# Kernel tuning notes

Measured on AMD Instinct MI355X. Metric: run time of the kernel, lower is better.

## Reference

```python
import jax, jax.numpy as jnp
import numpy as np

QUERY_DIM = 3072
HEADS = 24
HEAD_DIM = 128
INNER = HEADS * HEAD_DIM  # 3072
MLP_HIDDEN = int(QUERY_DIM * 4.0)  # 12288
MLP_MULT = 2
EPS = 1e-5
B, S = 1, 4096


def setup_inputs() -> dict:
    key = jax.random.key(0)
    ks = jax.random.split(key, 8)
    hidden_states = jax.random.normal(ks[0], (B, S, QUERY_DIM), dtype=jnp.float32)
    # rotary angles for half the head dim (interleaved / non-neox style)
    t = jnp.arange(S, dtype=jnp.float32)[:, None]
    inv_freq = 1.0 / (10000.0 ** (jnp.arange(0, HEAD_DIM, 2, dtype=jnp.float32) / HEAD_DIM))
    ang = t * inv_freq[None, :]
    cos = jnp.cos(ang)
    sin = jnp.sin(ang)
    W_qkv_mlp = jax.random.normal(ks[1], (QUERY_DIM, 3 * INNER + MLP_HIDDEN * MLP_MULT), dtype=jnp.float32) * 0.02
    W_out = jax.random.normal(ks[2], (INNER + MLP_HIDDEN, QUERY_DIM), dtype=jnp.float32) * 0.02
    b_out = jnp.zeros((QUERY_DIM,), dtype=jnp.float32)
    norm_q_w = jnp.ones((HEAD_DIM,), dtype=jnp.float32)
    norm_k_w = jnp.ones((HEAD_DIM,), dtype=jnp.float32)
    return {"hidden_states": hidden_states, "cos": cos, "sin": sin,
            "W_qkv_mlp": W_qkv_mlp, "W_out": W_out, "b_out": b_out,
            "norm_q_w": norm_q_w, "norm_k_w": norm_k_w}


def _rmsnorm(x, w, eps=EPS):
    var = jnp.mean(jnp.square(x), axis=-1, keepdims=True)
    return x * jax.lax.rsqrt(var + eps) * w


def _rope_interleaved(x, cos, sin):
    # x: [B,S,H,D]; cos/sin: [S, D//2]. Non-neox: rotate interleaved pairs.
    x1 = x[..., 0::2]
    x2 = x[..., 1::2]
    c = cos[None, :, None, :]
    s = sin[None, :, None, :]
    o1 = x1 * c - x2 * s
    o2 = x2 * c + x1 * s
    return jnp.stack([o1, o2], axis=-1).reshape(x.shape)


def reference(hidden_states, cos, sin, W_qkv_mlp, W_out, b_out, norm_q_w, norm_k_w):
    h = hidden_states @ W_qkv_mlp  # [B,S, 3*INNER + 2*MLP_HIDDEN]
    qkv, mlp = jnp.split(h, [3 * INNER], axis=-1)
    q, k, v = jnp.split(qkv, 3, axis=-1)
    q = q.reshape(B, S, HEADS, HEAD_DIM)
    k = k.reshape(B, S, HEADS, HEAD_DIM)
    v = v.reshape(B, S, HEADS, HEAD_DIM)
    q = _rmsnorm(q, norm_q_w)
    k = _rmsnorm(k, norm_k_w)
    q = _rope_interleaved(q, cos, sin)
    k = _rope_interleaved(k, cos, sin)
    scale = 1.0 / np.sqrt(HEAD_DIM)
    scores = jnp.einsum('bqhd,bkhd->bhqk', q, k) * scale
    probs = jax.nn.softmax(scores, axis=-1)
    attn = jnp.einsum('bhqk,bkhd->bqhd', probs, v)
    attn = attn.reshape(B, S, INNER)
    m1, m2 = jnp.split(mlp, 2, axis=-1)
    mlp_out = jax.nn.silu(m1) * m2
    out = jnp.concatenate([attn, mlp_out], axis=-1) @ W_out + b_out
    return out
```

## Files before the change

### kernel.cpp

```cpp
#include <hip/hip_runtime.h>

typedef short shortx8 __attribute__((ext_vector_type(8)));
typedef float floatx4 __attribute__((ext_vector_type(4)));
typedef unsigned short u16;

#define GLB(x) ((const __attribute__((address_space(1))) void*)(x))
#define LDSC(x) ((__attribute__((address_space(3))) void*)(x))
#define BAR() asm volatile("s_barrier" ::: "memory")
#define WAITV8() asm volatile("s_waitcnt vmcnt(8)" ::: "memory")

__device__ __forceinline__ float bf2f(u16 u) {
  unsigned x = ((unsigned)u) << 16;
  float f;
  __builtin_memcpy(&f, &x, 4);
  return f;
}
__device__ __forceinline__ u16 f2bf(float f) {
  unsigned x;
  __builtin_memcpy(&x, &f, 4);
  x += 0x7fffu + ((x >> 16) & 1u);
  return (u16)(x >> 16);
}

__global__ __launch_bounds__(256) void cast_bf16(const float* __restrict__ src,
                                                 u16* __restrict__ dst) {
  const size_t i = ((size_t)blockIdx.x * 256 + threadIdx.x) << 3;
  floatx4 a = *(const floatx4*)(src + i);
  floatx4 b = *(const floatx4*)(src + i + 4);
  shortx8 o;
#pragma unroll
  for (int e = 0; e < 4; ++e) {
    o[e] = (short)f2bf(a[e]);
    o[e + 4] = (short)f2bf(b[e]);
  }
  *(shortx8*)(dst + i) = o;
}

__global__ __launch_bounds__(256) void transpose_cast(const float* __restrict__ src,
                                                      u16* __restrict__ dst,
                                                      int R, int C, int perm) {
  __shared__ u16 T[64 * 72];
  const int tiles_c = C >> 6;
  const int r0 = (blockIdx.x / tiles_c) << 6;
  const int c0 = (blockIdx.x % tiles_c) << 6;
  const int tid = threadIdx.x;
  const int rl = tid >> 4;
  const int cb = (tid & 15) << 2;
#pragma unroll
  for (int rr = 0; rr < 4; ++rr) {
    const int row = rr * 16 + rl;
    floatx4 v = *(const floatx4*)(src + (size_t)(r0 + row) * C + c0 + cb);
#pragma unroll
    for (int i = 0; i < 4; ++i) T[(cb + i) * 72 + row] = f2bf(v[i]);
  }
  __syncthreads();
  int dbase = c0;
  if (perm && c0 >= 9216) {
    if (c0 < 21504) { const int u = c0 - 9216;  dbase = 9216 + ((u >> 7) << 8) + (u & 64); }
    else            { const int u = c0 - 21504; dbase = 9216 + ((u >> 7) << 8) + 128 + (u & 64); }
  }
#pragma unroll
  for (int ii = 0; ii < 2; ++ii) {
    const int chunk = tid + (ii << 8);
    const int cr = chunk >> 3;
    const int r8 = (chunk & 7) << 3;
    shortx8 v = *(const shortx8*)(T + cr * 72 + r8);
    *(shortx8*)(dst + (size_t)(dbase + cr) * R + r0 + r8) = v;
  }
}

template <int MODE>
__global__ __launch_bounds__(512, 2) void gemm8(const u16* __restrict__ A,
                                                const u16* __restrict__ B,
                                                void* __restrict__ Cout,
                                                u16* __restrict__ CC2,
                                                int M, int N, int K, int Ksub) {
  __shared__ u16 lds[8 * 8192];

  const int nbm = M >> 8;
  const int nwg = nbm * (N >> 8);
  const int cpx = nwg >> 3;
  const int wg = ((int)blockIdx.x & 7) * cpx + ((int)blockIdx.x >> 3);
  const int bm = wg % nbm;
  const int bn = wg / nbm;
  const int koff = (int)blockIdx.y * Ksub;

  const int tid = threadIdx.x;
  const int lane = tid & 63;
  const int w = tid >> 6;
  const int wm = w >> 2;
  const int wn = w & 3;
  const int l15 = lane & 15;
  const int l4 = lane >> 4;
  const int NT = Ksub >> 6;

  const int lrow = lane >> 2;
  const int lblk = lane & 3;

#define UNIT(buf, mat, ks) (lds + (((buf) * 4 + (mat) * 2 + (ks)) << 13))

  const u16* Abase = A + (size_t)bm * 256 * K + koff;
  const u16* Bbase = B + (size_t)bn * 256 * K + koff;

  auto STAGE = [&](int mat, int ks, int buf, int t) {
    const u16* gb = mat ? Bbase : Abase;
#pragma unroll
    for (int j = 0; j < 2; ++j) {
      const int row = (w * 2 + j) * 16 + lrow;
      const int sblk = lblk ^ ((row >> 1) & 3);
      const u16* src = gb + (size_t)row * K + (t << 6) + (ks << 5) + (sblk << 3);
      __builtin_amdgcn_global_load_lds(GLB(src),
                                       LDSC(UNIT(buf, mat, ks) + ((w * 2 + j) << 9)),
                                       16, 0, 0);
    }
  };
  auto LDA = [&](int mf, int ks, int buf) -> shortx8 {
    const int row = wm * 128 + mf * 16 + l15;
    return *(const shortx8*)(UNIT(buf, 0, ks) + row * 32 + ((l4 ^ ((row >> 1) & 3)) << 3));
  };
  auto LDB = [&](int nf, int ks, int buf) -> shortx8 {
    const int row = wn * 64 + nf * 16 + l15;
    return *(const shortx8*)(UNIT(buf, 1, ks) + row * 32 + ((l4 ^ ((row >> 1) & 3)) << 3));
  };

  floatx4 acc[8][4] = {};

  STAGE(0, 0, 0, 0); STAGE(1, 0, 0, 0);
  STAGE(0, 1, 0, 0); STAGE(1, 1, 0, 0);
  STAGE(0, 0, 1, 1); STAGE(1, 0, 1, 1);
  WAITV8();
  BAR();

#pragma unroll 2
  for (int T = 0; T < NT; ++T) {
    const int cur = T & 1, nxt = cur ^ 1;
    const int t1 = (T + 1 < NT) ? T + 1 : NT - 1;
    const int t2 = (T + 2 < NT) ? T + 2 : NT - 1;
    shortx8 af[4], bf[4];

#pragma unroll
    for (int m = 0; m < 4; ++m) af[m] = LDA(m, 0, cur);
#pragma unroll
    for (int n = 0; n < 4; ++n) bf[n] = LDB(n, 0, cur);
    STAGE(0, 1, nxt, t1);
    BAR();
    __builtin_amdgcn_s_setprio(1);
#pragma unroll
    for (int m = 0; m < 4; ++m)
#pragma unroll
      for (int n = 0; n < 4; ++n)
        acc[m][n] = __builtin_amdgcn_mfma_f32_16x16x32_bf16(af[m], bf[n], acc[m][n], 0, 0, 0);
    __builtin_amdgcn_s_setprio(0);
    BAR();

#pragma unroll
    for (int m = 0; m < 4; ++m) af[m] = LDA(4 + m, 0, cur);
    STAGE(1, 1, nxt, t1);
    BAR();
    __builtin_amdgcn_s_setprio(1);
#pragma unroll
    for (int m = 0; m < 4; ++m)
#pragma unroll
      for (int n = 0; n < 4; ++n)
        acc[4 + m][n] = __builtin_amdgcn_mfma_f32_16x16x32_bf16(af[m], bf[n], acc[4 + m][n], 0, 0, 0);
    __builtin_amdgcn_s_setprio(0);
    WAITV8();
    BAR();

#pragma unroll
    for (int m = 0; m < 4; ++m) af[m] = LDA(m, 1, cur);
#pragma unroll
    for (int n = 0; n < 4; ++n) bf[n] = LDB(n, 1, cur);
    STAGE(0, 0, cur, t2);
    BAR();
    __builtin_amdgcn_s_setprio(1);
#pragma unroll
    for (int m = 0; m < 4; ++m)
#pragma unroll
      for (int n = 0; n < 4; ++n)
        acc[m][n] = __builtin_amdgcn_mfma_f32_16x16x32_bf16(af[m], bf[n], acc[m][n], 0, 0, 0);
    __builtin_amdgcn_s_setprio(0);
    BAR();

#pragma unroll
    for (int m = 0; m < 4; ++m) af[m] = LDA(4 + m, 1, cur);
    STAGE(1, 0, cur, t2);
    BAR();
    __builtin_amdgcn_s_setprio(1);
#pragma unroll
    for (int m = 0; m < 4; ++m)
#pragma unroll
      for (int n = 0; n < 4; ++n)
        acc[4 + m][n] = __builtin_amdgcn_mfma_f32_16x16x32_bf16(af[m], bf[n], acc[4 + m][n], 0, 0, 0);
    __builtin_amdgcn_s_setprio(0);
    WAITV8();
    BAR();
  }

  const int orow0 = bm * 256 + wm * 128 + (l4 << 2);
  if (MODE == 0) {
    if (bn < 36) {
      u16* C = (u16*)Cout;
      const int ocol0 = bn * 256 + wn * 64 + l15;
#pragma unroll
      for (int m = 0; m < 8; ++m)
#pragma unroll
        for (int n = 0; n < 4; ++n)
#pragma unroll
          for (int r = 0; r < 4; ++r)
            C[(size_t)(orow0 + m * 16 + r) * 9216 + ocol0 + n * 16] = f2bf(acc[m][n][r]);
    } else {
      __syncthreads();
      float* buf = (float*)lds + (wm * 2 + (wn & 1)) * 8192;
      if (wn >= 2) {
#pragma unroll
        for (int m = 0; m < 8; ++m)
#pragma unroll
          for (int n = 0; n < 4; ++n) {
            const int col = n * 16 + l15;
            const int chunk = (m * 4 + l4) ^ (l15 & 7);
            *(floatx4*)(buf + ((col << 5) + chunk) * 4) = acc[m][n];
          }
      }
      __syncthreads();
      if (wn < 2) {
        const int gcol0 = 3072 + (bn - 36) * 128 + wn * 64 + l15;
#pragma unroll
        for (int m = 0; m < 8; ++m)
#pragma unroll
          for (int n = 0; n < 4; ++n) {
            const int col = n * 16 + l15;
            const int chunk = (m * 4 + l4) ^ (l15 & 7);
            const floatx4 m2v = *(const floatx4*)(buf + ((col << 5) + chunk) * 4);
#pragma unroll
            for (int r = 0; r < 4; ++r) {
              const float m1 = acc[m][n][r];
              const float sg = 1.0f / (1.0f + exp2f(-1.4426950408889634f * m1));
              CC2[(size_t)(orow0 + m * 16 + r) * 15360 + gcol0 + n * 16] =
                  f2bf(m1 * sg * m2v[r]);
            }
          }
      }
    }
  } else {
    float* C = (float*)Cout + (size_t)blockIdx.y * M * N;
    const int ocol0 = bn * 256 + wn * 64 + l15;
#pragma unroll
    for (int m = 0; m < 8; ++m)
#pragma unroll
      for (int n = 0; n < 4; ++n)
#pragma unroll
        for (int r = 0; r < 4; ++r)
          C[(size_t)(orow0 + m * 16 + r) * N + ocol0 + n * 16] = acc[m][n][r];
  }
}
#undef UNIT

__global__ __launch_bounds__(256) void reduce_bias(const float* __restrict__ P,
                                                   const float* __restrict__ bias,
                                                   float* __restrict__ out) {
  const size_t base = ((size_t)blockIdx.x * 256 + threadIdx.x) << 2;
  const size_t stride = (size_t)4096 * 3072;
  floatx4 a = *(const floatx4*)(P + base);
  floatx4 b = *(const floatx4*)(P + stride + base);
  floatx4 c = *(const floatx4*)(P + 2 * stride + base);
  floatx4 d = *(const floatx4*)(P + 3 * stride + base);
  floatx4 bb = *(const floatx4*)(bias + (base % 3072));
  *(floatx4*)(out + base) = a + b + c + d + bb;
}

#define QSCALE (0.08838834764831845f * 1.4426950408889634f)

__global__ __launch_bounds__(256, 2) void qkv_prep(
    const u16* __restrict__ H, const float* __restrict__ cosb,
    const float* __restrict__ sinb, const float* __restrict__ nqw,
    const float* __restrict__ nkw, u16* __restrict__ Qo, u16* __restrict__ Ko,
    u16* __restrict__ Vo) {
  __shared__ u16 VT[128 * 72];
  const int head = blockIdx.y;
  const int t0 = blockIdx.x << 6;
  const int tid = threadIdx.x;
  const int tl = tid >> 2;
  const int db = (tid & 3) << 5;
  const int token = t0 + tl;

  const u16* hp = H + (size_t)token * 9216 + head * 128 + db;
  shortx8 qv[4], kvv[4], vv[4];
#pragma unroll
  for (int i = 0; i < 4; ++i) {
    qv[i] = *(const shortx8*)(hp + i * 8);
    kvv[i] = *(const shortx8*)(hp + 3072 + i * 8);
    vv[i] = *(const shortx8*)(hp + 6144 + i * 8);
  }
  float qx[32], kx[32];
  float sq = 0.f, sk = 0.f;
#pragma unroll
  for (int i = 0; i < 4; ++i)
#pragma unroll
    for (int j = 0; j < 8; ++j) {
      float a = bf2f((u16)qv[i][j]); qx[i * 8 + j] = a; sq += a * a;
      float b = bf2f((u16)kvv[i][j]); kx[i * 8 + j] = b; sk += b * b;
    }
  sq += __shfl_xor(sq, 1); sq += __shfl_xor(sq, 2);
  sk += __shfl_xor(sk, 1); sk += __shfl_xor(sk, 2);
  const float rq = rsqrtf(sq * (1.0f / 128.0f) + 1e-5f);
  const float rk = rsqrtf(sk * (1.0f / 128.0f) + 1e-5f);

  shortx8 oqv[4], okv[4];
#pragma unroll
  for (int p = 0; p < 16; ++p) {
    const float c = cosb[(size_t)token * 64 + (db >> 1) + p];
    const float s = sinb[(size_t)token * 64 + (db >> 1) + p];
    const int vi = p >> 2, vj = (p & 3) << 1;
    float a1 = qx[2 * p] * rq * nqw[db + 2 * p];
    float a2 = qx[2 * p + 1] * rq * nqw[db + 2 * p + 1];
    oqv[vi][vj] = (short)f2bf((a1 * c - a2 * s) * QSCALE);
    oqv[vi][vj + 1] = (short)f2bf((a2 * c + a1 * s) * QSCALE);
    float b1 = kx[2 * p] * rk * nkw[db + 2 * p];
    float b2 = kx[2 * p + 1] * rk * nkw[db + 2 * p + 1];
    okv[vi][vj] = (short)f2bf(b1 * c - b2 * s);
    okv[vi][vj + 1] = (short)f2bf(b2 * c + b1 * s);
  }
  {
    u16* qo = Qo + (size_t)head * 4096 * 128 + (size_t)token * 128 + db;
    u16* ko = Ko + (size_t)head * 4096 * 128 + (size_t)token * 128 + db;
#pragma unroll
    for (int i = 0; i < 4; ++i) {
      *(shortx8*)(qo + i * 8) = oqv[i];
      *(shortx8*)(ko + i * 8) = okv[i];
    }
  }
#pragma unroll
  for (int i = 0; i < 4; ++i)
#pragma unroll
    for (int j = 0; j < 8; ++j) VT[(db + i * 8 + j) * 72 + tl] = (u16)vv[i][j];
  __syncthreads();
#pragma unroll
  for (int ii = 0; ii < 4; ++ii) {
    const int chunk = tid + (ii << 8);
    const int d = chunk >> 3;
    const int j8 = (chunk & 7) << 3;
    shortx8 v = *(const shortx8*)(VT + d * 72 + j8);
    *(shortx8*)(Vo + (size_t)head * 128 * 4096 + (size_t)d * 4096 + t0 + j8) = v;
  }
}

__global__ __launch_bounds__(256, 2) void attn_kernel(const u16* __restrict__ Qg,
                                                      const u16* __restrict__ Kg,
                                                      const u16* __restrict__ Vg,
                                                      u16* __restrict__ CC) {
  __shared__ u16 Ks[128 * 128];
  __shared__ u16 Vs[128 * 128];
  __shared__ u16 Ps[4 * 16 * 128];

  const int head = blockIdx.y;
  const int q0 = blockIdx.x << 6;
  const int tid = threadIdx.x;
  const int lane = tid & 63;
  const int wave = tid >> 6;
  const int l15 = lane & 15;
  const int l4 = lane >> 4;

  const u16* Qh = Qg + (size_t)head * 4096 * 128;
  const u16* Kh = Kg + (size_t)head * 4096 * 128;
  const u16* Vh = Vg + (size_t)head * 128 * 4096;

  shortx8 qf[4];
  {
    const u16* qp = Qh + (size_t)(q0 + wave * 16 + l15) * 128 + l4 * 8;
#pragma unroll
    for (int ks = 0; ks < 4; ++ks) qf[ks] = *(const shortx8*)(qp + ks * 32);
  }

  floatx4 o[8] = {};
  float mrun[4], lrun[4];
#pragma unroll
  for (int r = 0; r < 4; ++r) { mrun[r] = -1e30f; lrun[r] = 0.0f; }

  u16* Pw = Ps + wave * 2048;
  const int swz = l15 & 7;

  for (int s0 = 0; s0 < 4096; s0 += 128) {
#pragma unroll
    for (int i = 0; i < 8; ++i) {
      const int c = wave * 8 + i;
      const int row = c * 4 + (lane >> 4);
      const int blk = (lane & 15) ^ (row & 7);
      __builtin_amdgcn_global_load_lds(GLB(Kh + (size_t)(s0 + row) * 128 + blk * 8),
                                       LDSC(Ks + c * 512), 16, 0, 0);
    }
#pragma unroll
    for (int i = 0; i < 8; ++i) {
      const int c = wave * 8 + i;
      const int row = c * 4 + (lane >> 4);
      const int blk = (lane & 15) ^ (row & 7);
      __builtin_amdgcn_global_load_lds(GLB(Vh + (size_t)row * 4096 + s0 + blk * 8),
                                       LDSC(Vs + c * 512), 16, 0, 0);
    }
    __syncthreads();

    floatx4 s[8];
    __builtin_amdgcn_s_setprio(1);
#pragma unroll
    for (int n = 0; n < 8; ++n) {
      const int krow = n * 16 + l15;
      floatx4 acc = {};
#pragma unroll
      for (int ks = 0; ks < 4; ++ks) {
        shortx8 kf = *(const shortx8*)(Ks + krow * 128 + (((ks * 4 + l4) ^ swz) << 3));
        acc = __builtin_amdgcn_mfma_f32_16x16x32_bf16(qf[ks], kf, acc, 0, 0, 0);
      }
      s[n] = acc;
    }
    __builtin_amdgcn_s_setprio(0);

    float alpha[4];
#pragma unroll
    for (int r = 0; r < 4; ++r) {
      float v = fmaxf(fmaxf(fmaxf(s[0][r], s[1][r]), fmaxf(s[2][r], s[3][r])),
                      fmaxf(fmaxf(s[4][r], s[5][r]), fmaxf(s[6][r], s[7][r])));
      v = fmaxf(v, __shfl_xor(v, 1));
      v = fmaxf(v, __shfl_xor(v, 2));
      v = fmaxf(v, __shfl_xor(v, 4));
      v = fmaxf(v, __shfl_xor(v, 8));
      const float mn = fmaxf(mrun[r], v);
      alpha[r] = exp2f(mrun[r] - mn);
      mrun[r] = mn;
    }

    float rs[4] = {0.f, 0.f, 0.f, 0.f};
#pragma unroll
    for (int n = 0; n < 8; ++n) {
#pragma unroll
      for (int r = 0; r < 4; ++r) {
        const float p = exp2f(s[n][r] - mrun[r]);
        rs[r] += p;
        const int prow = (l4 << 2) + r;
        const int pblk = ((n << 1) + (l15 >> 3)) ^ (prow & 7);
        Pw[prow * 128 + (pblk << 3) + (l15 & 7)] = f2bf(p);
      }
    }
#pragma unroll
    for (int r = 0; r < 4; ++r) {
      float v = rs[r];
      v += __shfl_xor(v, 1);
      v += __shfl_xor(v, 2);
      v += __shfl_xor(v, 4);
      v += __shfl_xor(v, 8);
      lrun[r] = lrun[r] * alpha[r] + v;
    }
    if (__any((alpha[0] < 1.0f) || (alpha[1] < 1.0f) ||
              (alpha[2] < 1.0f) || (alpha[3] < 1.0f))) {
#pragma unroll
      for (int nd = 0; nd < 8; ++nd)
#pragma unroll
        for (int r = 0; r < 4; ++r) o[nd][r] *= alpha[r];
    }

    shortx8 pf[4];
#pragma unroll
    for (int ks = 0; ks < 4; ++ks)
      pf[ks] = *(const shortx8*)(Pw + l15 * 128 + (((ks * 4 + l4) ^ swz) << 3));
    __builtin_amdgcn_s_setprio(1);
#pragma unroll
    for (int nd = 0; nd < 8; ++nd) {
      const int vrow = nd * 16 + l15;
#pragma unroll
      for (int ks = 0; ks < 4; ++ks) {
        shortx8 vf = *(const shortx8*)(Vs + vrow * 128 + (((ks * 4 + l4) ^ swz) << 3));
        o[nd] = __builtin_amdgcn_mfma_f32_16x16x32_bf16(pf[ks], vf, o[nd], 0, 0, 0);
      }
    }
    __builtin_amdgcn_s_setprio(0);
    __syncthreads();
  }

#pragma unroll
  for (int r = 0; r < 4; ++r) {
    const float inv = 1.0f / lrun[r];
    const int row = q0 + wave * 16 + (l4 << 2) + r;
    u16* outp = CC + (size_t)row * 15360 + head * 128 + l15;
#pragma unroll
    for (int nd = 0; nd < 8; ++nd) outp[nd << 4] = f2bf(o[nd][r] * inv);
  }
}

extern "C" void kernel_launch(void* const* d_in, const int* in_sizes, int n_in,
                              void* d_out, int out_size, void* d_ws, size_t ws_size,
                              hipStream_t stream) {
  const float* hs = (const float*)d_in[0];
  const float* cosb = (const float*)d_in[1];
  const float* sinb = (const float*)d_in[2];
  const float* w1 = (const float*)d_in[3];
  const float* wout = (const float*)d_in[4];
  const float* bout = (const float*)d_in[5];
  const float* nqw = (const float*)d_in[6];
  const float* nkw = (const float*)d_in[7];
  float* out = (float*)d_out;

  char* ws = (char*)d_ws;
  u16* X16 = (u16*)ws; ws += (size_t)4096 * 3072 * 2;
  u16* W1T = (u16*)ws; ws += (size_t)33792 * 3072 * 2;
  u16* WOT = (u16*)ws; ws += (size_t)3072 * 15360 * 2;
  u16* H   = (u16*)ws; ws += (size_t)4096 * 33792 * 2;
  u16* Qb  = (u16*)ws; ws += (size_t)24 * 4096 * 128 * 2;
  u16* Kb  = (u16*)ws; ws += (size_t)24 * 4096 * 128 * 2;
  u16* VTb = (u16*)ws; ws += (size_t)24 * 4096 * 128 * 2;
  u16* CC  = (u16*)ws; ws += (size_t)4096 * 15360 * 2;
  float* Pk = (float*)H;

  cast_bf16<<<6144, 256, 0, stream>>>(hs, X16);
  transpose_cast<<<(3072 / 64) * (33792 / 64), 256, 0, stream>>>(w1, W1T, 3072, 33792, 1);
  transpose_cast<<<(15360 / 64) * (3072 / 64), 256, 0, stream>>>(wout, WOT, 15360, 3072, 0);
  gemm8<0><<<(4096 / 256) * (33792 / 256), 512, 0, stream>>>(X16, W1T, H, CC,
                                                             4096, 33792, 3072, 3072);
  qkv_prep<<<dim3(64, 24), 256, 0, stream>>>(H, cosb, sinb, nqw, nkw, Qb, Kb, VTb);
  attn_kernel<<<dim3(64, 24), 256, 0, stream>>>(Qb, Kb, VTb, CC);
  gemm8<1><<<dim3((4096 / 256) * (3072 / 256), 4), 512, 0, stream>>>(
      CC, WOT, Pk, nullptr, 4096, 3072, 15360, 3840);
  reduce_bias<<<(4096 * 3072 / 4) / 256, 256, 0, stream>>>(Pk, bout, out);
}
```

Measured before the change: 1.927 ms.

## Rewrite attention with 32x32 MFMA transposed scores and register-resident P

The attention kernel now uses 32x32x16 bf16 MFMA with K as the A operand, so each lane owns one query row's scores. P stays in registers, packed with v_cvt_pk_bf16 and exchanged across half-waves via shuffles, instead of going through LDS. Each block covers 128 queries, halving the grid and doubling K/V reuse, and the softmax reductions drop to a single cross-half shuffle. The SwiGLU epilogue in the first GEMM now splits the work so all four waves compute outputs over half the rows each, instead of two waves idling. The trade-off is higher register pressure and fewer blocks for occupancy.

```diff
diff --git a/kernel.cpp b/kernel.cpp
--- a/kernel.cpp
+++ b/kernel.cpp
@@ -1,8 +1,11 @@
 #include <hip/hip_runtime.h>
 
 typedef short shortx8 __attribute__((ext_vector_type(8)));
+typedef short shortx4 __attribute__((ext_vector_type(4)));
 typedef float floatx4 __attribute__((ext_vector_type(4)));
+typedef float floatx16 __attribute__((ext_vector_type(16)));
 typedef unsigned short u16;
+typedef unsigned int u32;
 
 #define GLB(x) ((const __attribute__((address_space(1))) void*)(x))
 #define LDSC(x) ((__attribute__((address_space(3))) void*)(x))
@@ -20,6 +23,11 @@
   __builtin_memcpy(&x, &f, 4);
   x += 0x7fffu + ((x >> 16) & 1u);
   return (u16)(x >> 16);
+}
+__device__ __forceinline__ u32 pk_bf16(float lo, float hi) {
+  u32 r;
+  asm("v_cvt_pk_bf16_f32 %0, %1, %2" : "=v"(r) : "v"(lo), "v"(hi));
+  return r;
 }
 
 __global__ __launch_bounds__(256) void cast_bf16(const float* __restrict__ src,
@@ -214,30 +222,51 @@
       float* buf = (float*)lds + (wm * 2 + (wn & 1)) * 8192;
       if (wn >= 2) {
 #pragma unroll
-        for (int m = 0; m < 8; ++m)
+        for (int m = 0; m < 4; ++m)
 #pragma unroll
           for (int n = 0; n < 4; ++n) {
-            const int col = n * 16 + l15;
             const int chunk = (m * 4 + l4) ^ (l15 & 7);
-            *(floatx4*)(buf + ((col << 5) + chunk) * 4) = acc[m][n];
+            *(floatx4*)(buf + (((n * 16 + l15) << 4) + chunk) * 4) = acc[m][n];
+          }
+      } else {
+#pragma unroll
+        for (int m = 0; m < 4; ++m)
+#pragma unroll
+          for (int n = 0; n < 4; ++n) {
+            const int chunk = (m * 4 + l4) ^ (l15 & 7);
+            *(floatx4*)(buf + 4096 + (((n * 16 + l15) << 4) + chunk) * 4) = acc[4 + m][n];
           }
       }
       __syncthreads();
+      const int gcol0 = 3072 + (bn - 36) * 128 + (wn & 1) * 64 + l15;
       if (wn < 2) {
-        const int gcol0 = 3072 + (bn - 36) * 128 + wn * 64 + l15;
-#pragma unroll
-        for (int m = 0; m < 8; ++m)
+#pragma unroll
+        for (int m = 0; m < 4; ++m)
 #pragma unroll
           for (int n = 0; n < 4; ++n) {
-            const int col = n * 16 + l15;
             const int chunk = (m * 4 + l4) ^ (l15 & 7);
-            const floatx4 m2v = *(const floatx4*)(buf + ((col << 5) + chunk) * 4);
+            const floatx4 m2v = *(const floatx4*)(buf + (((n * 16 + l15) << 4) + chunk) * 4);
 #pragma unroll
             for (int r = 0; r < 4; ++r) {
               const float m1 = acc[m][n][r];
               const float sg = 1.0f / (1.0f + exp2f(-1.4426950408889634f * m1));
               CC2[(size_t)(orow0 + m * 16 + r) * 15360 + gcol0 + n * 16] =
                   f2bf(m1 * sg * m2v[r]);
+            }
+          }
+      } else {
+#pragma unroll
+        for (int m = 0; m < 4; ++m)
+#pragma unroll
+          for (int n = 0; n < 4; ++n) {
+            const int chunk = (m * 4 + l4) ^ (l15 & 7);
+            const floatx4 m1v = *(const floatx4*)(buf + 4096 + (((n * 16 + l15) << 4) + chunk) * 4);
+#pragma unroll
+            for (int r = 0; r < 4; ++r) {
+              const float m1 = m1v[r];
+              const float sg = 1.0f / (1.0f + exp2f(-1.4426950408889634f * m1));
+              CC2[(size_t)(orow0 + (4 + m) * 16 + r) * 15360 + gcol0 + n * 16] =
+                  f2bf(m1 * sg * acc[4 + m][n][r]);
             }
           }
       }
@@ -351,34 +380,27 @@
                                                       u16* __restrict__ CC) {
   __shared__ u16 Ks[128 * 128];
   __shared__ u16 Vs[128 * 128];
-  __shared__ u16 Ps[4 * 16 * 128];
 
   const int head = blockIdx.y;
-  const int q0 = blockIdx.x << 6;
+  const int q0 = blockIdx.x << 7;
   const int tid = threadIdx.x;
   const int lane = tid & 63;
   const int wave = tid >> 6;
-  const int l15 = lane & 15;
-  const int l4 = lane >> 4;
+  const int l31 = lane & 31;
+  const int kh = lane >> 5;
 
   const u16* Qh = Qg + (size_t)head * 4096 * 128;
   const u16* Kh = Kg + (size_t)head * 4096 * 128;
   const u16* Vh = Vg + (size_t)head * 128 * 4096;
 
-  shortx8 qf[4];
-  {
-    const u16* qp = Qh + (size_t)(q0 + wave * 16 + l15) * 128 + l4 * 8;
-#pragma unroll
-    for (int ks = 0; ks < 4; ++ks) qf[ks] = *(const shortx8*)(qp + ks * 32);
-  }
-
-  floatx4 o[8] = {};
-  float mrun[4], lrun[4];
-#pragma unroll
-  for (int r = 0; r < 4; ++r) { mrun[r] = -1e30f; lrun[r] = 0.0f; }
-
-  u16* Pw = Ps + wave * 2048;
-  const int swz = l15 & 7;
+  const int qrow = q0 + wave * 32 + l31;
+  shortx8 qf[8];
+#pragma unroll
+  for (int ks = 0; ks < 8; ++ks)
+    qf[ks] = *(const shortx8*)(Qh + (size_t)qrow * 128 + ks * 16 + kh * 8);
+
+  floatx16 ot[4] = {};
+  float mrun = -1e30f, lrun = 0.0f;
 
   for (int s0 = 0; s0 < 4096; s0 += 128) {
 #pragma unroll
@@ -399,90 +421,96 @@
     }
     __syncthreads();
 
-    floatx4 s[8];
+    floatx16 st[4] = {};
     __builtin_amdgcn_s_setprio(1);
 #pragma unroll
-    for (int n = 0; n < 8; ++n) {
-      const int krow = n * 16 + l15;
-      floatx4 acc = {};
-#pragma unroll
-      for (int ks = 0; ks < 4; ++ks) {
-        shortx8 kf = *(const shortx8*)(Ks + krow * 128 + (((ks * 4 + l4) ^ swz) << 3));
-        acc = __builtin_amdgcn_mfma_f32_16x16x32_bf16(qf[ks], kf, acc, 0, 0, 0);
+    for (int kvt = 0; kvt < 4; ++kvt) {
+      const int krow = kvt * 32 + l31;
+#pragma unroll
+      for (int ks = 0; ks < 8; ++ks) {
+        shortx8 kf = *(const shortx8*)(Ks + krow * 128 + (((ks * 2 + kh) ^ (krow & 7)) << 3));
+        st[kvt] = __builtin_amdgcn_mfma_f32_32x32x16_bf16(kf, qf[ks], st[kvt], 0, 0, 0);
       }
-      s[n] = acc;
     }
     __builtin_amdgcn_s_setprio(0);
 
-    float alpha[4];
-#pragma unroll
-    for (int r = 0; r < 4; ++r) {
-      float v = fmaxf(fmaxf(fmaxf(s[0][r], s[1][r]), fmaxf(s[2][r], s[3][r])),
-                      fmaxf(fmaxf(s[4][r], s[5][r]), fmaxf(s[6][r], s[7][r])));
-      v = fmaxf(v, __shfl_xor(v, 1));
-      v = fmaxf(v, __shfl_xor(v, 2));
-      v = fmaxf(v, __shfl_xor(v, 4));
-      v = fmaxf(v, __shfl_xor(v, 8));
-      const float mn = fmaxf(mrun[r], v);
-      alpha[r] = exp2f(mrun[r] - mn);
-      mrun[r] = mn;
-    }
-
-    float rs[4] = {0.f, 0.f, 0.f, 0.f};
-#pragma unroll
-    for (int n = 0; n < 8; ++n) {
-#pragma unroll
-      for (int r = 0; r < 4; ++r) {
-        const float p = exp2f(s[n][r] - mrun[r]);
-        rs[r] += p;
-        const int prow = (l4 << 2) + r;
-        const int pblk = ((n << 1) + (l15 >> 3)) ^ (prow & 7);
-        Pw[prow * 128 + (pblk << 3) + (l15 & 7)] = f2bf(p);
+    float vmax = st[0][0];
+#pragma unroll
+    for (int t = 0; t < 4; ++t)
+#pragma unroll
+      for (int r = 0; r < 16; ++r) vmax = fmaxf(vmax, st[t][r]);
+    vmax = fmaxf(vmax, __shfl_xor(vmax, 32));
+    const float mn = fmaxf(mrun, vmax);
+    const float alpha = exp2f(mrun - mn);
+    mrun = mn;
+
+    float rs = 0.0f;
+#pragma unroll
+    for (int t = 0; t < 4; ++t)
+#pragma unroll
+      for (int r = 0; r < 16; ++r) {
+        const float p = exp2f(st[t][r] - mn);
+        st[t][r] = p;
+        rs += p;
       }
-    }
-#pragma unroll
-    for (int r = 0; r < 4; ++r) {
-      float v = rs[r];
-      v += __shfl_xor(v, 1);
-      v += __shfl_xor(v, 2);
-      v += __shfl_xor(v, 4);
-      v += __shfl_xor(v, 8);
-      lrun[r] = lrun[r] * alpha[r] + v;
-    }
-    if (__any((alpha[0] < 1.0f) || (alpha[1] < 1.0f) ||
-              (alpha[2] < 1.0f) || (alpha[3] < 1.0f))) {
-#pragma unroll
-      for (int nd = 0; nd < 8; ++nd)
-#pragma unroll
-        for (int r = 0; r < 4; ++r) o[nd][r] *= alpha[r];
-    }
-
-    shortx8 pf[4];
-#pragma unroll
-    for (int ks = 0; ks < 4; ++ks)
-      pf[ks] = *(const shortx8*)(Pw + l15 * 128 + (((ks * 4 + l4) ^ swz) << 3));
-    __builtin_amdgcn_s_setprio(1);
-#pragma unroll
-    for (int nd = 0; nd < 8; ++nd) {
-      const int vrow = nd * 16 + l15;
-#pragma unroll
-      for (int ks = 0; ks < 4; ++ks) {
-        shortx8 vf = *(const shortx8*)(Vs + vrow * 128 + (((ks * 4 + l4) ^ swz) << 3));
-        o[nd] = __builtin_amdgcn_mfma_f32_16x16x32_bf16(pf[ks], vf, o[nd], 0, 0, 0);
+    rs += __shfl_xor(rs, 32);
+    lrun = lrun * alpha + rs;
+    if (__any(alpha < 1.0f)) {
+#pragma unroll
+      for (int dt = 0; dt < 4; ++dt)
+#pragma unroll
+        for (int r = 0; r < 16; ++r) ot[dt][r] *= alpha;
+    }
+
+    u32 w[4][8];
+#pragma unroll
+    for (int t = 0; t < 4; ++t)
+#pragma unroll
+      for (int q = 0; q < 4; ++q) {
+        w[t][2 * q] = pk_bf16(st[t][4 * q], st[t][4 * q + 1]);
+        w[t][2 * q + 1] = pk_bf16(st[t][4 * q + 2], st[t][4 * q + 3]);
       }
-    }
-    __builtin_amdgcn_s_setprio(0);
+
+#pragma unroll
+    for (int ks = 0; ks < 8; ++ks) {
+      const int kvt = ks >> 1;
+      const int qA = 2 * (ks & 1);
+      const u32 wA0 = w[kvt][2 * qA], wA1 = w[kvt][2 * qA + 1];
+      const u32 wB0 = w[kvt][2 * qA + 2], wB1 = w[kvt][2 * qA + 3];
+      const u32 send0 = kh ? wA0 : wB0;
+      const u32 send1 = kh ? wA1 : wB1;
+      const u32 r0 = (u32)__shfl_xor((int)send0, 32);
+      const u32 r1 = (u32)__shfl_xor((int)send1, 32);
+      u32 fw[4];
+      fw[0] = kh ? r0 : wA0;
+      fw[1] = kh ? r1 : wA1;
+      fw[2] = kh ? wB0 : r0;
+      fw[3] = kh ? wB1 : r1;
+      shortx8 pf;
+      __builtin_memcpy(&pf, fw, 16);
+      __builtin_amdgcn_s_setprio(1);
+#pragma unroll
+      for (int dt = 0; dt < 4; ++dt) {
+        const int vrow = dt * 32 + l31;
+        shortx8 vf = *(const shortx8*)(Vs + vrow * 128 + (((ks * 2 + kh) ^ (vrow & 7)) << 3));
+        ot[dt] = __builtin_amdgcn_mfma_f32_32x32x16_bf16(vf, pf, ot[dt], 0, 0, 0);
+      }
+      __builtin_amdgcn_s_setprio(0);
+    }
     __syncthreads();
   }
 
-#pragma unroll
-  for (int r = 0; r < 4; ++r) {
-    const float inv = 1.0f / lrun[r];
-    const int row = q0 + wave * 16 + (l4 << 2) + r;
-    u16* outp = CC + (size_t)row * 15360 + head * 128 + l15;
-#pragma unroll
-    for (int nd = 0; nd < 8; ++nd) outp[nd << 4] = f2bf(o[nd][r] * inv);
-  }
+  const float inv = 1.0f / lrun;
+  u16* outp = CC + (size_t)qrow * 15360 + head * 128;
+#pragma unroll
+  for (int dt = 0; dt < 4; ++dt)
+#pragma unroll
+    for (int g = 0; g < 4; ++g) {
+      shortx4 pack;
+#pragma unroll
+      for (int r = 0; r < 4; ++r) pack[r] = (short)f2bf(ot[dt][4 * g + r] * inv);
+      *(shortx4*)(outp + dt * 32 + g * 8 + kh * 4) = pack;
+    }
 }
 
 extern "C" void kernel_launch(void* const* d_in, const int* in_sizes, int n_in,
@@ -515,7 +543,7 @@
   gemm8<0><<<(4096 / 256) * (33792 / 256), 512, 0, stream>>>(X16, W1T, H, CC,
                                                              4096, 33792, 3072, 3072);
   qkv_prep<<<dim3(64, 24), 256, 0, stream>>>(H, cosb, sinb, nqw, nkw, Qb, Kb, VTb);
-  attn_kernel<<<dim3(64, 24), 256, 0, stream>>>(Qb, Kb, VTb, CC);
+  attn_kernel<<<dim3(32, 24), 256, 0, stream>>>(Qb, Kb, VTb, CC);
   gemm8<1><<<dim3((4096 / 256) * (3072 / 256), 4), 512, 0, stream>>>(
       CC, WOT, Pk, nullptr, 4096, 3072, 15360, 3840);
   reduce_bias<<<(4096 * 3072 / 4) / 256, 256, 0, stream>>>(Pk, bout, out);
```

After: 1.759 ms. 8.7% less time.
